# Performance work log

Hardware: AMD Instinct MI355X
Metric: run time of the kernel (lower is better)

## Reference

```python
import jax, jax.numpy as jnp
import numpy as np

HEAD_NUM = 16
NEG_BIG = 1e12


def setup_inputs() -> dict:
    key = jax.random.key(0)
    ks = jax.random.split(key, 10)
    B, S, H = 4, 2048, 1024
    std = 0.02
    return {
        "encoder_outputs": jax.random.normal(ks[0], (B, S, H), dtype=jnp.float32),
        "mask": jax.random.randint(ks[1], (B, S), 0, 2, dtype=jnp.int32),
        "Wq": jax.random.normal(ks[2], (H, H), dtype=jnp.float32) * std,
        "bq": jax.random.normal(ks[3], (H,), dtype=jnp.float32) * std,
        "Wk": jax.random.normal(ks[4], (H, H), dtype=jnp.float32) * std,
        "bk": jax.random.normal(ks[5], (H,), dtype=jnp.float32) * std,
        "Wv": jax.random.normal(ks[6], (H, H), dtype=jnp.float32) * std,
        "bv": jax.random.normal(ks[7], (H,), dtype=jnp.float32) * std,
        "Wc": jax.random.normal(ks[8], (H, H), dtype=jnp.float32) * std,
    }


def _split_heads(x, h):
    # chunk(h, -1) + stack(dim=0): [B,S,H] -> [h,B,S,H//h]
    B, S, H = x.shape
    return jnp.moveaxis(x.reshape(B, S, h, H // h), 2, 0)


def reference(encoder_outputs, mask, Wq, bq, Wk, bk, Wv, bv, Wc):
    x = encoder_outputs
    B, S, H = x.shape
    hd = H // HEAD_NUM
    q = _split_heads(x @ Wq.T + bq, HEAD_NUM)  # [h,B,S,hd]
    k = _split_heads(x @ Wk.T + bk, HEAD_NUM)
    v = _split_heads(x @ Wv.T + bv, HEAD_NUM)
    dots = jnp.einsum("hbqd,hbkd->hbqk", q, k) / jnp.sqrt(jnp.float32(hd))
    m = mask.astype(jnp.float32)  # [B,S]; 0 = valid token
    inv = 1.0 - m
    eye = jnp.eye(S, dtype=jnp.float32)
    # clamp_max(1 - (1-m)_i (1-m)_j + eye, 1): [B,S,S]
    new_mask = jnp.minimum(1.0 - inv[:, :, None] * inv[:, None, :] + eye, 1.0)
    energies = dots - new_mask[None] * NEG_BIG
    weights = jax.nn.softmax(energies, axis=-1) * (1.0 - new_mask)[None]
    out = jnp.einsum("hbqk,hbkd->hbqd", weights, v)  # [h,B,S,hd]
    out = jnp.moveaxis(out, 0, 2).reshape(B, S, H)  # concat heads
    return out @ Wc.T
```

## Files before the change

kernel.cpp:

```cpp
#include <hip/hip_runtime.h>
#include <cstddef>
#include <cstdint>

#define BB 4
#define SS 2048
#define HH 1024
#define NH 16
#define HD 64

typedef _Float16 half8 __attribute__((ext_vector_type(8)));
typedef _Float16 half4v __attribute__((ext_vector_type(4)));
typedef float f32x4 __attribute__((ext_vector_type(4)));

#define KSCALE 0.1803368801111f

__device__ __forceinline__ void gload_lds16(const _Float16* g, char* l) {
    __builtin_amdgcn_global_load_lds(
        (const __attribute__((address_space(1))) void*)g,
        (__attribute__((address_space(3))) void*)l, 16, 0, 0);
}

__global__ __launch_bounds__(256)
void scan_mask(const int* __restrict__ mk, int* __restrict__ vidx, int* __restrict__ cnt)
{
    __shared__ int ps[256];
    const int b = blockIdx.x, t = threadIdx.x;
    int flag[8], s = 0;
#pragma unroll
    for (int k = 0; k < 8; ++k) { flag[k] = (mk[(b << 11) + t * 8 + k] == 0); s += flag[k]; }
    ps[t] = s;
    __syncthreads();
    for (int off = 1; off < 256; off <<= 1) {
        const int add = (t >= off) ? ps[t - off] : 0;
        __syncthreads();
        ps[t] += add;
        __syncthreads();
    }
    int pos = ps[t] - s;
#pragma unroll
    for (int k = 0; k < 8; ++k)
        if (flag[k]) vidx[(b << 11) + pos++] = t * 8 + k;
    if (t == 255) cnt[b] = ps[255];
}

__global__ __launch_bounds__(256)
void gather_x(const float* __restrict__ x, const int* __restrict__ vidx,
              const int* __restrict__ cnt, _Float16* __restrict__ xc)
{
    const int row = blockIdx.x;
    const int b = row >> 11, i = row & 2047;
    const int t = threadIdx.x;
    half4v hv = (half4v){0, 0, 0, 0};
    if (i < cnt[b]) {
        const float4 v = ((const float4*)(x + (size_t)((b << 11) + vidx[row]) * HH))[t];
        hv[0] = (_Float16)v.x; hv[1] = (_Float16)v.y;
        hv[2] = (_Float16)v.z; hv[3] = (_Float16)v.w;
    }
    ((half4v*)(xc + (size_t)row * HH))[t] = hv;
}

__global__ __launch_bounds__(256)
void cvt_w(const float* __restrict__ Wq, const float* __restrict__ Wk,
           const float* __restrict__ Wv, const float* __restrict__ Wc,
           _Float16* __restrict__ o)
{
    const float* src = blockIdx.z == 0 ? Wq : blockIdx.z == 1 ? Wk :
                       blockIdx.z == 2 ? Wv : Wc;
    _Float16* dst = o + (size_t)blockIdx.z * (HH * HH);
    const int i = blockIdx.x * 256 + threadIdx.x;
    const float4 v0 = ((const float4*)src)[(size_t)i * 2];
    const float4 v1 = ((const float4*)src)[(size_t)i * 2 + 1];
    half8 hv;
    hv[0] = (_Float16)v0.x; hv[1] = (_Float16)v0.y;
    hv[2] = (_Float16)v0.z; hv[3] = (_Float16)v0.w;
    hv[4] = (_Float16)v1.x; hv[5] = (_Float16)v1.y;
    hv[6] = (_Float16)v1.z; hv[7] = (_Float16)v1.w;
    ((half8*)dst)[i] = hv;
}

__device__ __forceinline__ void gemm_core(const _Float16* __restrict__ A,
                                          const _Float16* __restrict__ W,
                                          int K, int m0, int n0,
                                          char* As, char* Bs, f32x4 acc[4][4])
{
    const int t = threadIdx.x;
    const int w = t >> 6, lane = t & 63;
    const int ln = lane & 15, g = lane >> 4;
    const int wr = w >> 1, wc = w & 1;

    const int rr0 = w * 16 + (lane >> 2);
    const int rr1 = rr0 + 64;
    const int p   = lane & 3;
    const int sl0 = p ^ ((rr0 >> 1) & 3);
    const int sl1 = p ^ ((rr1 >> 1) & 3);
    const _Float16* ga0 = A + (size_t)(m0 + rr0) * K + sl0 * 8;
    const _Float16* ga1 = A + (size_t)(m0 + rr1) * K + sl1 * 8;
    const _Float16* gb0 = W + (size_t)(n0 + rr0) * K + sl0 * 8;
    const _Float16* gb1 = W + (size_t)(n0 + rr1) * K + sl1 * 8;
    char* dA = As + w * 1024 + lane * 16;
    char* dB = Bs + w * 1024 + lane * 16;

    int offA[4], offB[4];
#pragma unroll
    for (int i = 0; i < 4; ++i) {
        const int ra = wr * 64 + i * 16 + ln;
        offA[i] = ra * 64 + ((g ^ ((ra >> 1) & 3)) << 4);
        const int rb = wc * 64 + i * 16 + ln;
        offB[i] = rb * 64 + ((g ^ ((rb >> 1) & 3)) << 4);
    }

#pragma unroll
    for (int i = 0; i < 4; ++i)
#pragma unroll
        for (int j = 0; j < 4; ++j) acc[i][j] = (f32x4){0.f, 0.f, 0.f, 0.f};

    gload_lds16(ga0, dA);
    gload_lds16(ga1, dA + 4096);
    gload_lds16(gb0, dB);
    gload_lds16(gb1, dB + 4096);
    gload_lds16(ga0 + 32, dA + 8192);
    gload_lds16(ga1 + 32, dA + 8192 + 4096);
    gload_lds16(gb0 + 32, dB + 8192);
    gload_lds16(gb1 + 32, dB + 8192 + 4096);

    const int ns = K / 32;
    for (int k = 0; k < ns; ++k) {
        if (k < ns - 1) { asm volatile("s_waitcnt vmcnt(4)" ::: "memory"); }
        else            { asm volatile("s_waitcnt vmcnt(0)" ::: "memory"); }
        __builtin_amdgcn_s_barrier();
        __builtin_amdgcn_sched_barrier(0);

        const char* Ab = As + ((k & 1) << 13);
        const char* Bb = Bs + ((k & 1) << 13);
        half8 af[4], bf[4];
#pragma unroll
        for (int i = 0; i < 4; ++i) af[i] = *(const half8*)(Ab + offA[i]);
#pragma unroll
        for (int j = 0; j < 4; ++j) bf[j] = *(const half8*)(Bb + offB[j]);

        asm volatile("s_waitcnt lgkmcnt(0)" ::: "memory");
        __builtin_amdgcn_s_barrier();
        __builtin_amdgcn_sched_barrier(0);

        if (k + 2 < ns) {
            const int nb = (k & 1) << 13;
            const int ko = (k + 2) * 32;
            gload_lds16(ga0 + ko, dA + nb);
            gload_lds16(ga1 + ko, dA + nb + 4096);
            gload_lds16(gb0 + ko, dB + nb);
            gload_lds16(gb1 + ko, dB + nb + 4096);
        }
#pragma unroll
        for (int i = 0; i < 4; ++i)
#pragma unroll
            for (int j = 0; j < 4; ++j)
                acc[i][j] = __builtin_amdgcn_mfma_f32_16x16x32_f16(af[i], bf[j], acc[i][j], 0, 0, 0);
    }
}

__global__ __launch_bounds__(256)
void gemm_qkv(const _Float16* __restrict__ xc,
              const _Float16* __restrict__ Wq16, const _Float16* __restrict__ Wk16,
              const _Float16* __restrict__ Wv16,
              const float* __restrict__ bq, const float* __restrict__ bk,
              const float* __restrict__ bv, const int* __restrict__ cnt,
              _Float16* __restrict__ Qh, _Float16* __restrict__ Kh,
              _Float16* __restrict__ Vt)
{
    const int m0 = blockIdx.y * 128;
    const int bI = m0 >> 11;
    if ((m0 & 2047) >= ((cnt[bI] + 127) & ~127)) return;

    __shared__ __align__(16) char As[16384];
    __shared__ __align__(16) char Bs[16384];
    const int z = blockIdx.z;
    const _Float16* W = (z == 0) ? Wq16 : (z == 1) ? Wk16 : Wv16;
    const float* bias = (z == 0) ? bq : (z == 1) ? bk : bv;
    const int n0 = blockIdx.x * 128;

    f32x4 acc[4][4];
    gemm_core(xc, W, HH, m0, n0, As, Bs, acc);

    const int t = threadIdx.x;
    const int w = t >> 6, lane = t & 63;
    const int ln = lane & 15, g = lane >> 4;
    const int wr = w >> 1, wc = w & 1;
    const int mBase = m0 + wr * 64 + g * 4;
    const int nBase = n0 + wc * 64 + ln;

    if (z < 2) {
        _Float16* O = z ? Kh : Qh;
        const float sc = z ? 1.0f : KSCALE;
#pragma unroll
        for (int j = 0; j < 4; ++j) {
            const int n = nBase + j * 16;
            const int h = n >> 6, d = n & 63;
            const float bvf = bias[n];
#pragma unroll
            for (int i = 0; i < 4; ++i) {
                const int m = mBase + i * 16;
                const int b = m >> 11, s = m & 2047;
                _Float16* dst = O + (((size_t)(b * NH + h) * SS + s) * HD + d);
#pragma unroll
                for (int r = 0; r < 4; ++r)
                    dst[(size_t)r * HD] = (_Float16)((acc[i][j][r] + bvf) * sc);
            }
        }
    } else {
#pragma unroll
        for (int j = 0; j < 4; ++j) {
            const int n = nBase + j * 16;
            const int h = n >> 6, d = n & 63;
            const float bvf = bias[n];
#pragma unroll
            for (int i = 0; i < 4; ++i) {
                const int m = mBase + i * 16;
                const int b = m >> 11, s = m & 2047;
                const int sp = (s & ~31) | (((s >> 2) & 3) << 3) | (((s >> 4) & 1) << 2);
                half4v v;
#pragma unroll
                for (int r = 0; r < 4; ++r) v[r] = (_Float16)(acc[i][j][r] + bvf);
                *(half4v*)(Vt + ((size_t)(b * NH + h) * HD + d) * SS + sp) = v;
            }
        }
    }
}

__global__ __launch_bounds__(256)
void gemm_out(const _Float16* __restrict__ Oc, const _Float16* __restrict__ Wc16,
              const int* __restrict__ cnt, const int* __restrict__ vidx,
              float* __restrict__ C)
{
    const int m0 = blockIdx.y * 128;
    const int bI = m0 >> 11;
    const int cb = cnt[bI];
    if ((m0 & 2047) >= ((cb + 127) & ~127)) return;

    __shared__ __align__(16) char As[16384];
    __shared__ __align__(16) char Bs[16384];
    const int n0 = blockIdx.x * 128;

    f32x4 acc[4][4];
    gemm_core(Oc, Wc16, HH, m0, n0, As, Bs, acc);

    const int t = threadIdx.x;
    const int w = t >> 6, lane = t & 63;
    const int ln = lane & 15, g = lane >> 4;
    const int wr = w >> 1, wc = w & 1;
    const int mBase = m0 + wr * 64 + g * 4;
    const int nBase = n0 + wc * 64 + ln;
#pragma unroll
    for (int i = 0; i < 4; ++i) {
#pragma unroll
        for (int r = 0; r < 4; ++r) {
            const int m = mBase + i * 16 + r;
            const int lm = m & 2047;
            if (lm < cb) {
                const int orig = vidx[m];
                const size_t off = (size_t)((m & ~2047) + orig) * HH + nBase;
#pragma unroll
                for (int j = 0; j < 4; ++j)
                    C[off + j * 16] = acc[i][j][r];
            }
        }
    }
}

__global__ __launch_bounds__(512, 4)
void attn_mfma(const _Float16* __restrict__ Qh, const _Float16* __restrict__ Kh,
               const _Float16* __restrict__ Vt, const int* __restrict__ cnt,
               _Float16* __restrict__ Oc)
{
    __shared__ __align__(16) char ksm[3][8192];
    __shared__ __align__(16) char vsm[3][8192];

    const int t  = threadIdx.x;
    const int w  = t >> 6, l = t & 63, ln = l & 15, g = l >> 4;
    const int bh = blockIdx.x;
    const int b  = bh >> 4, h = bh & 15;
    const int cb = cnt[b];
    const int q0 = blockIdx.y << 6;
    if (q0 >= cb) return;
    const int p  = w & 3;
    const int hf = w >> 2;
    const int qw = q0 + (p << 4);
    const bool active = (qw < cb);
    const int nt = (cb + 63) >> 6;
    const int jtd = qw >> 6;
    const int rel = (qw & 63) + ln;

    half8 qf[2];
    f32x4 oacc[4];
    float lrun = 0.f;
    if (active) {
        const int qg = qw + ln;
        const _Float16* qp = Qh + ((size_t)bh * SS + qg) * HD + g * 8;
        qf[0] = *(const half8*)qp;
        qf[1] = *(const half8*)(qp + 32);
#pragma unroll
        for (int dd = 0; dd < 4; ++dd) oacc[dd] = (f32x4){0.f, 0.f, 0.f, 0.f};
    }

    const int sr = t >> 3;
    const int sl = (t & 7) ^ (sr & 7);
    const _Float16* kbase = Kh + ((size_t)bh * SS + sr) * HD + sl * 8;
    const _Float16* vbase = Vt + ((size_t)bh * HD + sr) * SS + sl * 8;

    gload_lds16(kbase, ksm[0] + t * 16);
    gload_lds16(vbase, vsm[0] + t * 16);
    if (nt > 1) {
        gload_lds16(kbase + (size_t)64 * HD, ksm[1] + t * 16);
        gload_lds16(vbase + 64,              vsm[1] + t * 16);
    }

    int cur = 0;
    for (int jt = 0; jt < nt; ++jt) {
        if (jt < nt - 1) { asm volatile("s_waitcnt vmcnt(2) lgkmcnt(0)" ::: "memory"); }
        else             { asm volatile("s_waitcnt vmcnt(0) lgkmcnt(0)" ::: "memory"); }
        __builtin_amdgcn_s_barrier();
        __builtin_amdgcn_sched_barrier(0);

        if (jt + 2 < nt) {
            const int nb = (cur + 2 >= 3) ? cur - 1 : cur + 2;
            const int jn = (jt + 2) << 6;
            gload_lds16(kbase + (size_t)jn * HD, ksm[nb] + t * 16);
            gload_lds16(vbase + jn,              vsm[nb] + t * 16);
        }

        if (active) {
            const int j0 = jt << 6;
            const char* kb = ksm[cur];
            const char* vb = vsm[cur];
            half8 kf[2][2];
#pragma unroll
            for (int tu = 0; tu < 2; ++tu) {
                const int row = (hf * 2 + tu) * 16 + ln;
                const int sw  = (row & 7) << 4;
                const int rb  = row * 128;
                kf[tu][0] = *(const half8*)(kb + ((rb + g * 16)      ^ sw));
                kf[tu][1] = *(const half8*)(kb + ((rb + 64 + g * 16) ^ sw));
            }
            const bool slow = (jt == jtd) | (j0 + 64 > cb);

            f32x4 sa[2];
            __builtin_amdgcn_s_setprio(1);
#pragma unroll
            for (int tu = 0; tu < 2; ++tu) {
                sa[tu] = (f32x4){0.f, 0.f, 0.f, 0.f};
                sa[tu] = __builtin_amdgcn_mfma_f32_16x16x32_f16(kf[tu][0], qf[0], sa[tu], 0, 0, 0);
                sa[tu] = __builtin_amdgcn_mfma_f32_16x16x32_f16(kf[tu][1], qf[1], sa[tu], 0, 0, 0);
            }
            __builtin_amdgcn_s_setprio(0);

            float wv[2][4];
#pragma unroll
            for (int tu = 0; tu < 2; ++tu)
#pragma unroll
                for (int r = 0; r < 4; ++r) {
                    float tv = sa[tu][r];
                    if (slow) {
                        const int kp = (hf * 2 + tu) * 16 + g * 4 + r;
                        if (((jt == jtd) & (kp == rel)) | (j0 + kp >= cb))
                            tv = -1e30f;
                    }
                    wv[tu][r] = exp2f(tv);
                }
            lrun += ((wv[0][0] + wv[0][1]) + (wv[0][2] + wv[0][3]))
                  + ((wv[1][0] + wv[1][1]) + (wv[1][2] + wv[1][3]));

            half8 pf;
            pf[0] = (_Float16)wv[0][0]; pf[1] = (_Float16)wv[0][1];
            pf[2] = (_Float16)wv[0][2]; pf[3] = (_Float16)wv[0][3];
            pf[4] = (_Float16)wv[1][0]; pf[5] = (_Float16)wv[1][1];
            pf[6] = (_Float16)wv[1][2]; pf[7] = (_Float16)wv[1][3];

            __builtin_amdgcn_s_setprio(1);
#pragma unroll
            for (int dd = 0; dd < 4; ++dd) {
                const int row = dd * 16 + ln;
                const int sw  = (row & 7) << 4;
                const int rb  = row * 128;
                const half8 vf = *(const half8*)(vb + ((rb + hf * 64 + g * 16) ^ sw));
                oacc[dd] = __builtin_amdgcn_mfma_f32_16x16x32_f16(vf, pf, oacc[dd], 0, 0, 0);
            }
            __builtin_amdgcn_s_setprio(0);
        }
        cur = (cur + 1 == 3) ? 0 : cur + 1;
    }

    __syncthreads();
    f32x4* cmo = (f32x4*)vsm;
    float* cml = (float*)(cmo + 1024);
    if (active && hf == 1) {
#pragma unroll
        for (int dd = 0; dd < 4; ++dd) cmo[(p * 4 + dd) * 64 + l] = oacc[dd];
        cml[p * 64 + l] = lrun;
    }
    __syncthreads();
    if (active && hf == 0) {
#pragma unroll
        for (int dd = 0; dd < 4; ++dd) oacc[dd] += cmo[(p * 4 + dd) * 64 + l];
        float ls = lrun + cml[p * 64 + l];
        ls += __shfl_xor(ls, 16);
        ls += __shfl_xor(ls, 32);
        const int iq = qw + ln;
        if (iq < cb) {
            const float inv = (ls > 0.f) ? 1.f / ls : 0.f;
            _Float16* op = Oc + ((size_t)((b << 11) + iq)) * HH + h * HD + g * 4;
#pragma unroll
            for (int dd = 0; dd < 4; ++dd) {
                half4v hv;
#pragma unroll
                for (int r = 0; r < 4; ++r) hv[r] = (_Float16)(oacc[dd][r] * inv);
                *(half4v*)(op + dd * 16) = hv;
            }
        }
    }
}

extern "C" void kernel_launch(void* const* d_in, const int* in_sizes, int n_in,
                              void* d_out, int out_size, void* d_ws, size_t ws_size,
                              hipStream_t stream)
{
    (void)in_sizes; (void)n_in; (void)ws_size;

    const float* x  = (const float*)d_in[0];
    const int*   mk = (const int*)d_in[1];
    const float* Wq = (const float*)d_in[2];
    const float* bq = (const float*)d_in[3];
    const float* Wk = (const float*)d_in[4];
    const float* bk = (const float*)d_in[5];
    const float* Wv = (const float*)d_in[6];
    const float* bv = (const float*)d_in[7];
    const float* Wc = (const float*)d_in[8];
    float* out = (float*)d_out;

    const int M = BB * SS;
    const size_t NE = (size_t)M * HH;
    const size_t NW = (size_t)HH * HH;
    _Float16* xc  = (_Float16*)d_ws;
    _Float16* W16 = xc + NE;
    _Float16* Qh  = W16 + 4 * NW;
    _Float16* Kh  = Qh + NE;
    _Float16* Vt  = Kh + NE;
    _Float16* Oc  = Vt + NE;
    int* vidx = (int*)(Oc + NE);
    int* cnt  = vidx + M;

    hipMemsetAsync(out, 0, (size_t)out_size * sizeof(float), stream);
    scan_mask<<<BB, 256, 0, stream>>>(mk, vidx, cnt);
    gather_x<<<M, 256, 0, stream>>>(x, vidx, cnt, xc);
    cvt_w<<<dim3(512, 1, 4), 256, 0, stream>>>(Wq, Wk, Wv, Wc, W16);

    dim3 gq(HH / 128, M / 128, 3);
    gemm_qkv<<<gq, 256, 0, stream>>>(xc, W16, W16 + NW, W16 + 2 * NW,
                                     bq, bk, bv, cnt, Qh, Kh, Vt);

    dim3 ga(BB * NH, SS / 64);
    attn_mfma<<<ga, 512, 0, stream>>>(Qh, Kh, Vt, cnt, Oc);

    dim3 go(HH / 128, M / 128);
    gemm_out<<<go, 256, 0, stream>>>(Oc, W16 + 3 * NW, cnt, vidx, out);
}
```

Measured before the change: 135.1 us.

## Triple-buffer GEMM LDS pipeline, zero only masked output rows, flatten QKV grid

The shared GEMM core moves from a double-buffered LDS pipeline with two barriers per K-step to a three-slot ring buffer with one barrier per step. The next tile's loads are issued before the current tile's LDS reads, so global loads overlap compute and one barrier is removed. The full-output memset is replaced by a kernel that zeroes only the rows of masked tokens, using an inverse index list that scan_mask now builds. The QKV GEMM grid is flattened so the z dimension becomes part of the column index over the contiguous weight buffer. LDS use per block rises from 32KB to 48KB, which may reduce occupancy.

After: 136.9 us. Within noise of the previous version (+1.3%).

```diff
diff --git a/kernel.cpp b/kernel.cpp
--- a/kernel.cpp
+++ b/kernel.cpp
@@ -21,7 +21,8 @@
 }
 
 __global__ __launch_bounds__(256)
-void scan_mask(const int* __restrict__ mk, int* __restrict__ vidx, int* __restrict__ cnt)
+void scan_mask(const int* __restrict__ mk, int* __restrict__ vidx,
+               int* __restrict__ ividx, int* __restrict__ cnt)
 {
     __shared__ int ps[256];
     const int b = blockIdx.x, t = threadIdx.x;
@@ -36,11 +37,26 @@
         ps[t] += add;
         __syncthreads();
     }
-    int pos = ps[t] - s;
-#pragma unroll
-    for (int k = 0; k < 8; ++k)
-        if (flag[k]) vidx[(b << 11) + pos++] = t * 8 + k;
+    int posv = ps[t] - s;
+#pragma unroll
+    for (int k = 0; k < 8; ++k) {
+        const int gidx = t * 8 + k;
+        if (flag[k]) vidx[(b << 11) + posv++] = gidx;
+        else         ividx[(b << 11) + (gidx - posv)] = gidx;
+    }
     if (t == 255) cnt[b] = ps[255];
+}
+
+__global__ __launch_bounds__(256)
+void zero_inv(const int* __restrict__ ividx, const int* __restrict__ cnt,
+              float* __restrict__ out)
+{
+    const int row = blockIdx.x;
+    const int b = row >> 11, i = row & 2047;
+    if (i < SS - cnt[b]) {
+        float* p = out + (size_t)((b << 11) + ividx[row]) * HH;
+        ((float4*)p)[threadIdx.x] = make_float4(0.f, 0.f, 0.f, 0.f);
+    }
 }
 
 __global__ __launch_bounds__(256)
@@ -124,44 +140,40 @@
     gload_lds16(gb1 + 32, dB + 8192 + 4096);
 
     const int ns = K / 32;
+    int cur = 0;
     for (int k = 0; k < ns; ++k) {
         if (k < ns - 1) { asm volatile("s_waitcnt vmcnt(4)" ::: "memory"); }
         else            { asm volatile("s_waitcnt vmcnt(0)" ::: "memory"); }
         __builtin_amdgcn_s_barrier();
         __builtin_amdgcn_sched_barrier(0);
 
-        const char* Ab = As + ((k & 1) << 13);
-        const char* Bb = Bs + ((k & 1) << 13);
-        half8 af[4], bf[4];
-#pragma unroll
-        for (int i = 0; i < 4; ++i) af[i] = *(const half8*)(Ab + offA[i]);
-#pragma unroll
-        for (int j = 0; j < 4; ++j) bf[j] = *(const half8*)(Bb + offB[j]);
-
-        asm volatile("s_waitcnt lgkmcnt(0)" ::: "memory");
-        __builtin_amdgcn_s_barrier();
-        __builtin_amdgcn_sched_barrier(0);
-
         if (k + 2 < ns) {
-            const int nb = (k & 1) << 13;
+            const int nbuf = (cur + 2 >= 3) ? cur - 1 : cur + 2;
+            const int nb = nbuf << 13;
             const int ko = (k + 2) * 32;
             gload_lds16(ga0 + ko, dA + nb);
             gload_lds16(ga1 + ko, dA + nb + 4096);
             gload_lds16(gb0 + ko, dB + nb);
             gload_lds16(gb1 + ko, dB + nb + 4096);
         }
+        const char* Ab = As + (cur << 13);
+        const char* Bb = Bs + (cur << 13);
+        half8 af[4], bf[4];
+#pragma unroll
+        for (int i = 0; i < 4; ++i) af[i] = *(const half8*)(Ab + offA[i]);
+#pragma unroll
+        for (int j = 0; j < 4; ++j) bf[j] = *(const half8*)(Bb + offB[j]);
 #pragma unroll
         for (int i = 0; i < 4; ++i)
 #pragma unroll
             for (int j = 0; j < 4; ++j)
                 acc[i][j] = __builtin_amdgcn_mfma_f32_16x16x32_f16(af[i], bf[j], acc[i][j], 0, 0, 0);
-    }
-}
-
-__global__ __launch_bounds__(256)
-void gemm_qkv(const _Float16* __restrict__ xc,
-              const _Float16* __restrict__ Wq16, const _Float16* __restrict__ Wk16,
-              const _Float16* __restrict__ Wv16,
+        cur = (cur + 1 == 3) ? 0 : cur + 1;
+    }
+}
+
+__global__ __launch_bounds__(256)
+void gemm_qkv(const _Float16* __restrict__ xc, const _Float16* __restrict__ W16,
               const float* __restrict__ bq, const float* __restrict__ bk,
               const float* __restrict__ bv, const int* __restrict__ cnt,
               _Float16* __restrict__ Qh, _Float16* __restrict__ Kh,
@@ -171,15 +183,14 @@
     const int bI = m0 >> 11;
     if ((m0 & 2047) >= ((cnt[bI] + 127) & ~127)) return;
 
-    __shared__ __align__(16) char As[16384];
-    __shared__ __align__(16) char Bs[16384];
-    const int z = blockIdx.z;
-    const _Float16* W = (z == 0) ? Wq16 : (z == 1) ? Wk16 : Wv16;
+    __shared__ __align__(16) char As[24576];
+    __shared__ __align__(16) char Bs[24576];
+    const int n0 = blockIdx.x * 128;
+    const int z = n0 >> 10;
     const float* bias = (z == 0) ? bq : (z == 1) ? bk : bv;
-    const int n0 = blockIdx.x * 128;
 
     f32x4 acc[4][4];
-    gemm_core(xc, W, HH, m0, n0, As, Bs, acc);
+    gemm_core(xc, W16, HH, m0, n0, As, Bs, acc);
 
     const int t = threadIdx.x;
     const int w = t >> 6, lane = t & 63;
@@ -193,9 +204,9 @@
         const float sc = z ? 1.0f : KSCALE;
 #pragma unroll
         for (int j = 0; j < 4; ++j) {
-            const int n = nBase + j * 16;
-            const int h = n >> 6, d = n & 63;
-            const float bvf = bias[n];
+            const int nn = (nBase + j * 16) & 1023;
+            const int h = nn >> 6, d = nn & 63;
+            const float bvf = bias[nn];
 #pragma unroll
             for (int i = 0; i < 4; ++i) {
                 const int m = mBase + i * 16;
@@ -209,9 +220,9 @@
     } else {
 #pragma unroll
         for (int j = 0; j < 4; ++j) {
-            const int n = nBase + j * 16;
-            const int h = n >> 6, d = n & 63;
-            const float bvf = bias[n];
+            const int nn = (nBase + j * 16) & 1023;
+            const int h = nn >> 6, d = nn & 63;
+            const float bvf = bias[nn];
 #pragma unroll
             for (int i = 0; i < 4; ++i) {
                 const int m = mBase + i * 16;
@@ -236,8 +247,8 @@
     const int cb = cnt[bI];
     if ((m0 & 2047) >= ((cb + 127) & ~127)) return;
 
-    __shared__ __align__(16) char As[16384];
-    __shared__ __align__(16) char Bs[16384];
+    __shared__ __align__(16) char As[24576];
+    __shared__ __align__(16) char Bs[24576];
     const int n0 = blockIdx.x * 128;
 
     f32x4 acc[4][4];
@@ -422,7 +433,7 @@
                               void* d_out, int out_size, void* d_ws, size_t ws_size,
                               hipStream_t stream)
 {
-    (void)in_sizes; (void)n_in; (void)ws_size;
+    (void)in_sizes; (void)n_in; (void)out_size; (void)ws_size;
 
     const float* x  = (const float*)d_in[0];
     const int*   mk = (const int*)d_in[1];
@@ -444,17 +455,17 @@
     _Float16* Kh  = Qh + NE;
     _Float16* Vt  = Kh + NE;
     _Float16* Oc  = Vt + NE;
-    int* vidx = (int*)(Oc + NE);
-    int* cnt  = vidx + M;
-
-    hipMemsetAsync(out, 0, (size_t)out_size * sizeof(float), stream);
-    scan_mask<<<BB, 256, 0, stream>>>(mk, vidx, cnt);
+    int* vidx  = (int*)(Oc + NE);
+    int* cnt   = vidx + M;
+    int* ividx = cnt + 64;
+
+    scan_mask<<<BB, 256, 0, stream>>>(mk, vidx, ividx, cnt);
+    zero_inv<<<M, 256, 0, stream>>>(ividx, cnt, out);
     gather_x<<<M, 256, 0, stream>>>(x, vidx, cnt, xc);
     cvt_w<<<dim3(512, 1, 4), 256, 0, stream>>>(Wq, Wk, Wv, Wc, W16);
 
-    dim3 gq(HH / 128, M / 128, 3);
-    gemm_qkv<<<gq, 256, 0, stream>>>(xc, W16, W16 + NW, W16 + 2 * NW,
-                                     bq, bk, bv, cnt, Qh, Kh, Vt);
+    dim3 gq(3 * HH / 128, M / 128);
+    gemm_qkv<<<gq, 256, 0, stream>>>(xc, W16, bq, bk, bv, cnt, Qh, Kh, Vt);
 
     dim3 ga(BB * NH, SS / 64);
     attn_mfma<<<ga, 512, 0, stream>>>(Qh, Kh, Vt, cnt, Oc);
```
